# Kernel optimization log

Hardware: AMD Instinct MI355X
Metric: run time of the kernel (lower is better)

The kernel has to match this reference:

```python
import jax, jax.numpy as jnp
import numpy as np
import math

DIM = 1024
ATTN_DIM = 1024
B, S = 2, 4096

def setup_inputs() -> dict:
    key = jax.random.key(0)
    k1, k2, k3 = jax.random.split(key, 3)
    x = jax.random.normal(k1, (B, S, DIM), dtype=jnp.float32)
    # qkv Linear(dim, 3*attn_dim, bias=True): weight [3*attn_dim, dim], bias [3*attn_dim]
    W_qkv = jax.random.normal(k2, (3 * ATTN_DIM, DIM), dtype=jnp.float32) * (1.0 / math.sqrt(DIM))
    b_qkv = jax.random.normal(k3, (3 * ATTN_DIM,), dtype=jnp.float32) * 0.01
    return {"x": x, "W_qkv": W_qkv, "b_qkv": b_qkv}

def reference(x, W_qkv, b_qkv):
    b, s, d = x.shape
    qkv = jnp.einsum('bsd,ed->bse', x, W_qkv) + b_qkv  # [B,S,3*attn_dim]
    q, k, v = jnp.split(qkv, 3, axis=-1)
    score = jnp.einsum('bqd,bkd->bqk', q, k)  # [B,S,S]
    # causal mask applied BEFORE scaling (matches original: -inf survives the divide)
    causal = jnp.tril(jnp.ones((s, s), dtype=bool))
    score = jnp.where(causal, score, -jnp.inf)
    attn = jax.nn.softmax(score / math.sqrt(ATTN_DIM), axis=-1)
    y = jnp.einsum('bqk,bkd->bqd', attn, v)  # [B,S,attn_dim]
    return y
```

## Files before the change

kernel.cpp:

```cpp
#include <hip/hip_runtime.h>
#include <cstdint>
#include <cstddef>

typedef __bf16 bf16;
typedef bf16 bf16x4 __attribute__((ext_vector_type(4)));
typedef bf16 bf16x8 __attribute__((ext_vector_type(8)));
typedef float f32x4 __attribute__((ext_vector_type(4)));

#define SEQ 4096
#define DIMD 1024
#define TILE_K1024 131072L
#define TILE_K4096 524288L
#define PC_BATCH   8650752L

__device__ __forceinline__ int swz(int r, int c) {
    return r * 32 + (((((c >> 3) ^ (r >> 1)) & 3)) << 3) + (c & 7);
}

__device__ __forceinline__ void async16(void* lds, const void* g) {
    __builtin_amdgcn_global_load_lds(
        (__attribute__((address_space(1))) void*)g,
        (__attribute__((address_space(3))) void*)lds,
        16, 0, 0);
}

__device__ __forceinline__ void gemm_core(
    const bf16* __restrict__ At, const bf16* __restrict__ Bt,
    int k0, int k1, f32x4 acc[4][4])
{
    __shared__ bf16 lB[4096];
    const int tid  = threadIdx.x;
    const int lane = tid & 63;
    const int wid  = tid >> 6;
    const int wm   = (wid >> 1) * 64;
    const int wn   = (wid & 1) * 64;
    const int lr   = lane & 15;
    const int q    = lane >> 4;

    int offA[4], offB[4];
#pragma unroll
    for (int mi = 0; mi < 4; ++mi) {
        const int rA = wm + mi * 16 + lr;
        offA[mi] = rA * 32 + ((((rA >> 1) ^ q) & 3) << 3);
    }
#pragma unroll
    for (int ni = 0; ni < 4; ++ni) {
        const int rB = wn + ni * 16 + lr;
        offB[ni] = rB * 32 + ((((rB >> 1) ^ q) & 3) << 3);
    }

    for (int kk = k0; kk < k1; ++kk) {
        const bf16* sa = At + (long)kk * 4096;
        const bf16* sb = Bt + (long)kk * 4096;
        bf16x8 af[4];
#pragma unroll
        for (int mi = 0; mi < 4; ++mi)
            af[mi] = *(const bf16x8*)(sa + offA[mi]);
        async16(&lB[tid * 8],        sb + tid * 8);
        async16(&lB[2048 + tid * 8], sb + 2048 + tid * 8);
        __syncthreads();

        bf16x8 bfr[4];
#pragma unroll
        for (int ni = 0; ni < 4; ++ni)
            bfr[ni] = *(const bf16x8*)&lB[offB[ni]];
#pragma unroll
        for (int mi = 0; mi < 4; ++mi)
#pragma unroll
            for (int ni = 0; ni < 4; ++ni)
                acc[mi][ni] = __builtin_amdgcn_mfma_f32_16x16x32_bf16(
                    af[mi], bfr[ni], acc[mi][ni], 0, 0, 0);
        __syncthreads();
    }
}

__global__ __launch_bounds__(256) void cvt_all_kernel(
    const float* __restrict__ x, const float* __restrict__ W,
    bf16* __restrict__ xt, bf16* __restrict__ wt, float* __restrict__ sums)
{
    const int g = blockIdx.x, tid = threadIdx.x;
    if (g >= 11264) { sums[(g - 11264) * 256 + tid] = 0.0f; return; }
    const float* in; bf16* out; int i;
    if (g < 8192) { in = x; out = xt; i = g * 256 + tid; }
    else          { in = W; out = wt; i = (g - 8192) * 256 + tid; }
    const float4 v = ((const float4*)in)[i];
    const int j = i * 4, row = j >> 10, col = j & 1023;
    const long o = (long)(row >> 7) * TILE_K1024 + (col >> 5) * 4096
                 + swz(row & 127, col & 31);
    bf16x4 ov = { (bf16)v.x, (bf16)v.y, (bf16)v.z, (bf16)v.w };
    *(bf16x4*)&out[o] = ov;
}

__global__ __launch_bounds__(256) void qkv_gemm(
    const bf16* __restrict__ xt, const bf16* __restrict__ wt,
    const float* __restrict__ bias,
    bf16* __restrict__ Qt, bf16* __restrict__ Kt, bf16* __restrict__ Vtt)
{
    const int b = blockIdx.x, x = b & 7, r = b >> 3;
    const int mt = x * 8 + r / 24, wnid = r % 24;
    const int bm = mt * 128, bn = wnid * 128;

    f32x4 acc[4][4] = {};
    gemm_core(xt + (long)mt * TILE_K1024, wt + (long)wnid * TILE_K1024, 0, 32, acc);

    const int tid = threadIdx.x, lane = tid & 63, wid = tid >> 6;
    const int wm = (wid >> 1) * 64, wn = (wid & 1) * 64;
    const int lr = lane & 15, q4 = (lane >> 4) * 4;
#pragma unroll
    for (int ni = 0; ni < 4; ++ni) {
        const int n = bn + wn + ni * 16 + lr;
        const float bv = bias[n];
#pragma unroll
        for (int mi = 0; mi < 4; ++mi) {
            const int m0 = bm + wm + mi * 16 + q4;
            if (n < 2048) {
                bf16* dst = (n < 1024) ? Qt : Kt;
                const int c = n & 1023;
#pragma unroll
                for (int rr = 0; rr < 4; ++rr) {
                    const int m = m0 + rr;
                    dst[(long)(m >> 7) * TILE_K1024 + (c >> 5) * 4096
                        + swz(m & 127, c & 31)] = (bf16)(acc[mi][ni][rr] + bv);
                }
            } else {
                const int bb = m0 >> 12, s = m0 & 4095, d = n - 2048;
                bf16x4 o = { (bf16)(acc[mi][ni][0] + bv), (bf16)(acc[mi][ni][1] + bv),
                             (bf16)(acc[mi][ni][2] + bv), (bf16)(acc[mi][ni][3] + bv) };
                *(bf16x4*)&Vtt[(long)bb * 4194304 + (long)(d >> 7) * TILE_K4096
                               + (s >> 5) * 4096 + swz(d & 127, s & 31)] = o;
            }
        }
    }
}

__global__ __launch_bounds__(256) void score_kernel(
    const bf16* __restrict__ Qt, const bf16* __restrict__ Kt,
    bf16* __restrict__ Pc, float* __restrict__ sums)
{
    const int b = blockIdx.x, x = b & 7;
    int r = b >> 3;
    const int bz = r / 66, batch = bz;
    r %= 66;
    int qt, kt;
    const int s0 = x + 1;
    if (r < s0)           { qt = x;      kt = r; }
    else if (r < 33)      { qt = 31 - x; kt = r - s0; }
    else if (r < 42 + x)  { qt = x + 8;  kt = r - 33; }
    else                  { qt = 23 - x; kt = r - 42 - x; }

    bf16* Pb = Pc + (long)bz * PC_BATCH + (long)(qt * (qt + 1) / 2 + kt) * 16384;
    float* sb = sums + (long)batch * SEQ;

    f32x4 acc[4][4] = {};
    gemm_core(Qt + (long)(batch * 32 + qt) * TILE_K1024,
              Kt + (long)(batch * 32 + kt) * TILE_K1024, 0, 32, acc);

    const int tid = threadIdx.x, lane = tid & 63, wid = tid >> 6;
    const int wm = (wid >> 1) * 64, wn = (wid & 1) * 64;
    const int lr = lane & 15, q4 = (lane >> 4) * 4;
#pragma unroll
    for (int mi = 0; mi < 4; ++mi) {
#pragma unroll
        for (int rr = 0; rr < 4; ++rr) {
            const int ql = wm + mi * 16 + q4 + rr;
            const int q  = qt * 128 + ql;
            float rsum = 0.0f;
#pragma unroll
            for (int ni = 0; ni < 4; ++ni) {
                const int kl  = wn + ni * 16 + lr;
                const int key = kt * 128 + kl;
                const float s = acc[mi][ni][rr] * 0.03125f;
                const float p = (key <= q) ? __expf(s) : 0.0f;
                const bf16 pb = (bf16)p;
                Pb[(kl >> 5) * 4096 + swz(ql, kl & 31)] = pb;
                rsum += (float)pb;
            }
            rsum += __shfl_xor(rsum, 1);
            rsum += __shfl_xor(rsum, 2);
            rsum += __shfl_xor(rsum, 4);
            rsum += __shfl_xor(rsum, 8);
            if (lr == 0) atomicAdd(&sb[q], rsum);
        }
    }
}

__device__ const unsigned char pv_sched[96] = {
     15, 125,  28,  44,  25,  54,  86,  51,  83, 112,   4,   3,
     47,  93,  60,  12,  57,  22, 118,  19, 115,  80,  36,  35,
     31,  61,  92, 122,  89, 119,  10,  41,  18,  48,   5,   2,
     63,  29, 124,  90, 121,  87,  42,   9,  50,  16,  37,  34,
     95,  46,  13,  58,  24,  55,  21, 116,  82, 113,   7,   0,
    127,  14,  45,  26,  56,  23,  53,  84, 114,  81,  39,  32,
     30, 126,  27, 123,  88,  43,  85,  52,   8,  49,   6,   1,
     62,  94,  59,  91, 120,  11, 117,  20,  40,  17,  38,  33,
};

__global__ __launch_bounds__(256) void pv_kernel(
    const bf16* __restrict__ Pc, const bf16* __restrict__ Vtt,
    const float* __restrict__ sums, float* __restrict__ Y,
    float* __restrict__ part)
{
    const int b = blockIdx.x, x = b & 7, t = b >> 3;
    const int j = t >> 3, dt = t & 7;
    const int e = pv_sched[x * 12 + j];
    const int qt = e & 31, bz = (e >> 5) & 1, c = e >> 6;
    const int full = (qt + 1) * 4, half = (qt + 1) * 2;
    int k0, k1;
    if (qt < 16) { k0 = 0; k1 = full; }
    else { k0 = c ? half : 0; k1 = c ? full : half; }
    const int batch = bz;

    f32x4 acc[4][4] = {};
    gemm_core(Pc + (long)bz * PC_BATCH + (long)(qt * (qt + 1) / 2) * 16384,
              Vtt + (long)batch * 4194304 + (long)dt * TILE_K4096, k0, k1, acc);

    const int tid = threadIdx.x, lane = tid & 63, wid = tid >> 6;
    const int wm = (wid >> 1) * 64, wn = (wid & 1) * 64;
    const int lr = lane & 15, q4 = (lane >> 4) * 4;
#pragma unroll
    for (int mi = 0; mi < 4; ++mi) {
#pragma unroll
        for (int rr = 0; rr < 4; ++rr) {
            const int q = qt * 128 + wm + mi * 16 + q4 + rr;
            const float iv = 1.0f / sums[(long)batch * SEQ + q];
#pragma unroll
            for (int ni = 0; ni < 4; ++ni) {
                const int d = dt * 128 + wn + ni * 16 + lr;
                const float v = acc[mi][ni][rr] * iv;
                if (c == 0)
                    Y[(long)batch * 4194304 + (long)q * DIMD + d] = v;
                else
                    part[(long)bz * 2097152 + (long)(q - 2048) * DIMD + d] = v;
            }
        }
    }
}

__global__ __launch_bounds__(256) void combine_kernel(
    float* __restrict__ Y, const float* __restrict__ part)
{
    const long g = (long)blockIdx.x * 256 + threadIdx.x;
    const long e4 = g * 4;
    const int bz = (int)(e4 >> 21);
    const long rem = e4 & 2097151;
    float4 a = *(const float4*)&Y[(long)bz * 4194304 + 2097152 + rem];
    const float4 p = *(const float4*)&part[e4];
    a.x += p.x; a.y += p.y; a.z += p.z; a.w += p.w;
    *(float4*)&Y[(long)bz * 4194304 + 2097152 + rem] = a;
}

extern "C" void kernel_launch(void* const* d_in, const int* in_sizes, int n_in,
                              void* d_out, int out_size, void* d_ws, size_t ws_size,
                              hipStream_t stream)
{
    const float* x    = (const float*)d_in[0];
    const float* W    = (const float*)d_in[1];
    const float* bqkv = (const float*)d_in[2];
    float* out = (float*)d_out;
    char* ws = (char*)d_ws;

    bf16* Pc   = (bf16*)ws;
    bf16* xt   = (bf16*)ws;
    bf16* wt   = (bf16*)(ws + 16 * 1024 * 1024);
    bf16* Kt   = (bf16*)(ws + 34603008);
    bf16* Vtt  = (bf16*)(ws + 51380224);
    float* sums = (float*)(ws + 68157440);
    bf16* Qt   = (bf16*)d_out;
    float* part = (float*)Kt;

    cvt_all_kernel<<<11296, 256, 0, stream>>>(x, W, xt, wt, sums);
    qkv_gemm<<<1536, 256, 0, stream>>>(xt, wt, bqkv, Qt, Kt, Vtt);
    score_kernel<<<1056, 256, 0, stream>>>(Qt, Kt, Pc, sums);
    pv_kernel<<<768, 256, 0, stream>>>(Pc, Vtt, sums, out, part);
    combine_kernel<<<4096, 256, 0, stream>>>(out, part);
}
```

Measured before the change: 268.7 us.

## Double-buffer A and B tiles in LDS with async prefetch in GEMM core

The GEMM core now stages both the A and B tiles into a two-slot LDS ring with global_load_lds, issuing the load for step k+2 while step k computes. Before, A was read directly from global memory into registers each step and B was loaded synchronously with two barriers. Manual vmcnt waits and raw barriers replace __syncthreads, and setprio raises wave priority around the MFMA block. The cost is four times the LDS (32 KB per block), which may reduce occupancy, and the hand-counted vmcnt is fragile if the compiler emits other vector memory ops.

```diff
diff --git a/kernel.cpp b/kernel.cpp
--- a/kernel.cpp
+++ b/kernel.cpp
@@ -28,7 +28,7 @@
     const bf16* __restrict__ At, const bf16* __restrict__ Bt,
     int k0, int k1, f32x4 acc[4][4])
 {
-    __shared__ bf16 lB[4096];
+    __shared__ bf16 lt[2][2][4096];
     const int tid  = threadIdx.x;
     const int lane = tid & 63;
     const int wid  = tid >> 6;
@@ -49,29 +49,48 @@
         offB[ni] = rB * 32 + ((((rB >> 1) ^ q) & 3) << 3);
     }
 
+    const int t8 = tid * 8;
+
+#define STAGE(kk, c) do { \
+        const bf16* _sa = At + (long)(kk) * 4096; \
+        const bf16* _sb = Bt + (long)(kk) * 4096; \
+        async16(&lt[c][0][t8],        _sa + t8); \
+        async16(&lt[c][0][2048 + t8], _sa + 2048 + t8); \
+        async16(&lt[c][1][t8],        _sb + t8); \
+        async16(&lt[c][1][2048 + t8], _sb + 2048 + t8); \
+    } while (0)
+
+    STAGE(k0, 0);
+    if (k0 + 1 < k1) STAGE(k0 + 1, 1);
+
     for (int kk = k0; kk < k1; ++kk) {
-        const bf16* sa = At + (long)kk * 4096;
-        const bf16* sb = Bt + (long)kk * 4096;
-        bf16x8 af[4];
+        const int cur = (kk - k0) & 1;
+        if (kk + 1 < k1) { asm volatile("s_waitcnt vmcnt(4)" ::: "memory"); }
+        else             { asm volatile("s_waitcnt vmcnt(0)" ::: "memory"); }
+        __builtin_amdgcn_s_barrier();
+        __builtin_amdgcn_sched_barrier(0);
+
+        bf16x8 af[4], bfr[4];
 #pragma unroll
         for (int mi = 0; mi < 4; ++mi)
-            af[mi] = *(const bf16x8*)(sa + offA[mi]);
-        async16(&lB[tid * 8],        sb + tid * 8);
-        async16(&lB[2048 + tid * 8], sb + 2048 + tid * 8);
-        __syncthreads();
-
-        bf16x8 bfr[4];
+            af[mi] = *(const bf16x8*)&lt[cur][0][offA[mi]];
 #pragma unroll
         for (int ni = 0; ni < 4; ++ni)
-            bfr[ni] = *(const bf16x8*)&lB[offB[ni]];
+            bfr[ni] = *(const bf16x8*)&lt[cur][1][offB[ni]];
+
+        __builtin_amdgcn_s_setprio(1);
 #pragma unroll
         for (int mi = 0; mi < 4; ++mi)
 #pragma unroll
             for (int ni = 0; ni < 4; ++ni)
                 acc[mi][ni] = __builtin_amdgcn_mfma_f32_16x16x32_bf16(
                     af[mi], bfr[ni], acc[mi][ni], 0, 0, 0);
-        __syncthreads();
-    }
+        __builtin_amdgcn_s_setprio(0);
+        __builtin_amdgcn_sched_barrier(0);
+        __builtin_amdgcn_s_barrier();
+        if (kk + 2 < k1) STAGE(kk + 2, cur);
+    }
+#undef STAGE
 }
 
 __global__ __launch_bounds__(256) void cvt_all_kernel(
```

Result: faster. 235.9 us (-12.2%).

## Double-buffer B tiles in LDS and prefetch A fragments in the GEMM core

Applied to the files above, without the earlier changes.

The GEMM main loop now keeps two LDS buffers for the B tile and issues the async global-to-LDS load for step k+2 while computing step k. The A register fragments for the next step are loaded before the current MFMAs, with explicit vmcnt waits, sched barriers and raised wave priority around the MFMA block. This is meant to hide global-load latency that the single-buffer loop exposed with two full barriers per step. It doubles LDS use for B and adds registers for the second A fragment set. The loop is unrolled by two, so it assumes an even number of k-steps, and it relies on hand-counted vmcnt values being correct.

```diff
diff --git a/kernel.cpp b/kernel.cpp
--- a/kernel.cpp
+++ b/kernel.cpp
@@ -28,7 +28,7 @@
     const bf16* __restrict__ At, const bf16* __restrict__ Bt,
     int k0, int k1, f32x4 acc[4][4])
 {
-    __shared__ bf16 lB[4096];
+    __shared__ bf16 lB[2][4096];
     const int tid  = threadIdx.x;
     const int lane = tid & 63;
     const int wid  = tid >> 6;
@@ -37,41 +37,71 @@
     const int lr   = lane & 15;
     const int q    = lane >> 4;
 
-    int offA[4], offB[4];
-#pragma unroll
-    for (int mi = 0; mi < 4; ++mi) {
-        const int rA = wm + mi * 16 + lr;
-        offA[mi] = rA * 32 + ((((rA >> 1) ^ q) & 3) << 3);
-    }
+    const int rA0 = wm + lr;
+    const bf16* ap = At + (long)k0 * 4096
+                   + rA0 * 32 + ((((rA0 >> 1) ^ q) & 3) << 3);
+
+    int offB[4];
 #pragma unroll
     for (int ni = 0; ni < 4; ++ni) {
         const int rB = wn + ni * 16 + lr;
         offB[ni] = rB * 32 + ((((rB >> 1) ^ q) & 3) << 3);
     }
 
-    for (int kk = k0; kk < k1; ++kk) {
-        const bf16* sa = At + (long)kk * 4096;
-        const bf16* sb = Bt + (long)kk * 4096;
-        bf16x8 af[4];
-#pragma unroll
-        for (int mi = 0; mi < 4; ++mi)
-            af[mi] = *(const bf16x8*)(sa + offA[mi]);
-        async16(&lB[tid * 8],        sb + tid * 8);
-        async16(&lB[2048 + tid * 8], sb + 2048 + tid * 8);
-        __syncthreads();
-
-        bf16x8 bfr[4];
-#pragma unroll
-        for (int ni = 0; ni < 4; ++ni)
-            bfr[ni] = *(const bf16x8*)&lB[offB[ni]];
-#pragma unroll
-        for (int mi = 0; mi < 4; ++mi)
-#pragma unroll
-            for (int ni = 0; ni < 4; ++ni)
-                acc[mi][ni] = __builtin_amdgcn_mfma_f32_16x16x32_bf16(
-                    af[mi], bfr[ni], acc[mi][ni], 0, 0, 0);
-        __syncthreads();
-    }
+    const int t8 = tid * 8;
+
+#define STAGEB(kk, c) do { \
+        const bf16* _sb = Bt + (long)(kk) * 4096; \
+        async16(&lB[c][t8],        _sb + t8); \
+        async16(&lB[c][2048 + t8], _sb + 2048 + t8); \
+    } while (0)
+
+#define LOADA(dst) do { \
+        dst[0] = *(const bf16x8*)(ap); \
+        dst[1] = *(const bf16x8*)(ap + 512); \
+        dst[2] = *(const bf16x8*)(ap + 1024); \
+        dst[3] = *(const bf16x8*)(ap + 1536); \
+        ap += 4096; \
+    } while (0)
+
+    bf16x8 afA[4], afB[4];
+
+    LOADA(afA);
+    __builtin_amdgcn_sched_barrier(0);
+    STAGEB(k0, 0);
+    if (k0 + 1 < k1) STAGEB(k0 + 1, 1);
+
+#define ITER(kk, cur, AFU, AFN) do { \
+    if ((kk) + 1 < k1) { asm volatile("s_waitcnt vmcnt(2)" ::: "memory"); } \
+    else               { asm volatile("s_waitcnt vmcnt(0)" ::: "memory"); } \
+    __builtin_amdgcn_s_barrier(); \
+    __builtin_amdgcn_sched_barrier(0); \
+    if ((kk) + 1 < k1) LOADA(AFN); \
+    __builtin_amdgcn_sched_barrier(0); \
+    bf16x8 bfr[4]; \
+    _Pragma("unroll") \
+    for (int ni = 0; ni < 4; ++ni) \
+        bfr[ni] = *(const bf16x8*)&lB[cur][offB[ni]]; \
+    __builtin_amdgcn_s_setprio(1); \
+    _Pragma("unroll") \
+    for (int mi = 0; mi < 4; ++mi) { \
+      _Pragma("unroll") \
+      for (int ni = 0; ni < 4; ++ni) \
+        acc[mi][ni] = __builtin_amdgcn_mfma_f32_16x16x32_bf16( \
+            AFU[mi], bfr[ni], acc[mi][ni], 0, 0, 0); } \
+    __builtin_amdgcn_s_setprio(0); \
+    __builtin_amdgcn_sched_barrier(0); \
+    __builtin_amdgcn_s_barrier(); \
+    if ((kk) + 2 < k1) STAGEB((kk) + 2, cur); \
+} while (0)
+
+    for (int kk = k0; kk < k1; kk += 2) {
+        ITER(kk,     0, afA, afB);
+        ITER(kk + 1, 1, afB, afA);
+    }
+#undef ITER
+#undef LOADA
+#undef STAGEB
 }
 
 __global__ __launch_bounds__(256) void cvt_all_kernel(
```

After: 262.4 us. 1.02x faster.
